# Kernel optimization log

Hardware: AMD Instinct MI355X
Metric: run time of the kernel (lower is better)

Reference implementation:

```python
import jax, jax.numpy as jnp
import numpy as np

D_CHAR, D_HID, LEN_VOC = 256, 1024, 512
BSZ, MAX_LEN = 128, 256


def setup_inputs() -> dict:
    key = jax.random.key(0)
    ks = jax.random.split(key, 14)
    s = 1.0 / np.sqrt(D_HID)  # PyTorch RNN/Linear init scale
    u = lambda k, shape: jax.random.uniform(k, shape, jnp.float32, -s, s)
    return {
        "inputs": jax.random.randint(ks[0], (BSZ, MAX_LEN), 0, LEN_VOC),
        "outputs": jax.random.randint(ks[1], (BSZ, MAX_LEN), 0, LEN_VOC),
        "emb": jax.random.normal(ks[2], (LEN_VOC, D_CHAR), jnp.float32),
        "enc_Wih": u(ks[3], (D_HID, D_CHAR)),
        "enc_Whh": u(ks[4], (D_HID, D_HID)),
        "enc_bih": u(ks[5], (D_HID,)),
        "enc_bhh": u(ks[6], (D_HID,)),
        "dec_Wih": u(ks[7], (D_HID, D_CHAR)),
        "dec_Whh": u(ks[8], (D_HID, D_HID)),
        "dec_bih": u(ks[9], (D_HID,)),
        "dec_bhh": u(ks[10], (D_HID,)),
        "out_W": u(ks[11], (LEN_VOC, D_HID)),
        "out_b": u(ks[12], (LEN_VOC,)),
    }


def rnn_scan(x_seq, h0, Wih, Whh, bih, bhh):
    """Elman RNN (tanh), batch_first input [B, T, D] -> (h_T [B,H], all h [T,B,H]).
    h_t = tanh(W_ih x_t + b_ih + W_hh h_{t-1} + b_hh), matching torch.nn.RNN."""
    # Precompute input projection for all timesteps (one big GEMM).
    xp = jnp.einsum('btd,hd->bth', x_seq, Wih) + bih + bhh  # [B,T,H]
    xp = jnp.swapaxes(xp, 0, 1)  # [T,B,H] for scan

    def step(h, x):
        h = jnp.tanh(x + h @ Whh.T)
        return h, h

    hT, hs = jax.lax.scan(step, h0, xp)
    return hT, hs


def reference(inputs, outputs, emb, enc_Wih, enc_Whh, enc_bih, enc_bhh,
              dec_Wih, dec_Whh, dec_bih, dec_bhh, out_W, out_b):
    bsz, max_len = inputs.shape
    # Encoder over input char embeddings, zero initial hidden.
    embs = emb[inputs]  # [B,T,Dc]
    h0 = jnp.zeros((bsz, D_HID), jnp.float32)
    hT, _ = rnn_scan(embs, h0, enc_Wih, enc_Whh, enc_bih, enc_bhh)
    # Teacher-forced decoder: step 0 gets zero input, step t gets emb(outputs[:, t-1]).
    dec_in = jnp.concatenate(
        [jnp.zeros((bsz, 1, D_CHAR), jnp.float32), emb[outputs[:, :-1]]], axis=1)
    _, dec_hs = rnn_scan(dec_in, hT, dec_Wih, dec_Whh, dec_bih, dec_bhh)  # [T,B,H]
    # decoder_states.transpose(0,1).view(-1, d_hid)
    states = jnp.swapaxes(dec_hs, 0, 1).reshape(-1, D_HID)  # [B*T, H]
    logits = states @ out_W.T + out_b  # [B*T, V]
    return jax.nn.log_softmax(logits, axis=1)
```

## Files before the change

### kernel.cpp

```cpp
#include <hip/hip_runtime.h>


typedef short short8 __attribute__((ext_vector_type(8)));
typedef float floatx4 __attribute__((ext_vector_type(4)));
typedef unsigned int uint4v __attribute__((ext_vector_type(4)));

#define WS_WIN    0ull
#define WS_STATES (2ull << 20)
#define WS_WB     (66ull << 20)

#define HS_STRIDE 1032

__device__ __forceinline__ float bf2f(unsigned short u) {
  union { unsigned u; float f; } x; x.u = ((unsigned)u) << 16; return x.f;
}
__device__ __forceinline__ unsigned short f2bf(float f) {
  union { float f; unsigned u; } x; x.f = f;
  unsigned r = x.u + 0x7FFFu + ((x.u >> 16) & 1u);
  return (unsigned short)(r >> 16);
}
__device__ __forceinline__ unsigned pkminu16(unsigned a, unsigned b) {
  unsigned d;
  asm("v_pk_min_u16 %0, %1, %2" : "=v"(d) : "v"(a), "v"(b));
  return d;
}

__global__ __launch_bounds__(256) void cvt_kernel(
    const float* __restrict__ src, unsigned short* __restrict__ dst, int n)
{
  const int i = (blockIdx.x * 256 + threadIdx.x) * 4;
  if (i >= n) return;
  const float4 v = *(const float4*)(src + i);
  unsigned short o[4] = {f2bf(v.x), f2bf(v.y), f2bf(v.z), f2bf(v.w)};
  *(uint2*)(dst + i) = *(const uint2*)o;
}

__global__ __launch_bounds__(256) void gemm_bt_kernel(
    const unsigned short* __restrict__ Abase,
    const int mode,
    const unsigned short* __restrict__ Bmat,
    const float* __restrict__ bias0,
    const float* __restrict__ bias1,
    unsigned short* __restrict__ outp_bf,
    float* __restrict__ outp_f,
    const int K, const int N, const int nbn)
{
  __shared__ unsigned short As[64][264];
  __shared__ unsigned short Bs[64][264];
  __shared__ const unsigned short* rowsrc[64];

  const int tid = threadIdx.x;
  const int lane = tid & 63;
  const int wave = tid >> 6;
  const int bn = blockIdx.x % nbn;
  const int bm = blockIdx.x / nbn;
  const int m0 = bm * 64;
  const int j0 = bn * 64;

  if (tid < 64) {
    const int m = m0 + tid;
    const unsigned short* src;
    if (mode == 0) {
      src = Abase + (size_t)m * K;
    } else {
      src = Abase + ((size_t)(m & 255) * 128 + (m >> 8)) * 1024;
    }
    rowsrc[tid] = src;
  }

  const floatx4 zf = {0.f, 0.f, 0.f, 0.f};
  floatx4 acc0 = zf, acc1 = zf, acc2 = zf, acc3 = zf;

  for (int kc = 0; kc < K; kc += 256) {
    __syncthreads();
#pragma unroll
    for (int i = 0; i < 8; ++i) {
      const int idx = i * 256 + tid;
      const int r = idx >> 5;
      const int c = idx & 31;
      const unsigned short* s = rowsrc[r];
      *(short8*)&As[r][c * 8] = *(const short8*)(s + kc + c * 8);
      *(short8*)&Bs[r][c * 8] =
          *(const short8*)(Bmat + (size_t)(j0 + r) * K + kc + c * 8);
    }
    __syncthreads();
    const int ar = 16 * wave + (lane & 15);
    const int kq = (lane >> 4) * 8;
#pragma unroll
    for (int kk = 0; kk < 8; ++kk) {
      const short8 a = *(const short8*)&As[ar][kk * 32 + kq];
      const short8 bv0 = *(const short8*)&Bs[(lane & 15)][kk * 32 + kq];
      acc0 = __builtin_amdgcn_mfma_f32_16x16x32_bf16(a, bv0, acc0, 0, 0, 0);
      const short8 bv1 = *(const short8*)&Bs[16 + (lane & 15)][kk * 32 + kq];
      acc1 = __builtin_amdgcn_mfma_f32_16x16x32_bf16(a, bv1, acc1, 0, 0, 0);
      const short8 bv2 = *(const short8*)&Bs[32 + (lane & 15)][kk * 32 + kq];
      acc2 = __builtin_amdgcn_mfma_f32_16x16x32_bf16(a, bv2, acc2, 0, 0, 0);
      const short8 bv3 = *(const short8*)&Bs[48 + (lane & 15)][kk * 32 + kq];
      acc3 = __builtin_amdgcn_mfma_f32_16x16x32_bf16(a, bv3, acc3, 0, 0, 0);
    }
  }

  float bs[4] = {0.f, 0.f, 0.f, 0.f};
  if (bias0) {
#pragma unroll
    for (int nt = 0; nt < 4; ++nt) {
      const int jj = j0 + nt * 16 + (lane & 15);
      bs[nt] = bias0[jj] + bias1[jj];
    }
  }
  __syncthreads();
  const int rbase = 16 * wave + (lane >> 4) * 4;
  const int cl = lane & 15;

  if (outp_bf) {
#pragma unroll
    for (int i = 0; i < 4; ++i) {
      As[rbase + i][cl]      = f2bf(acc0[i] + bs[0]);
      As[rbase + i][16 + cl] = f2bf(acc1[i] + bs[1]);
      As[rbase + i][32 + cl] = f2bf(acc2[i] + bs[2]);
      As[rbase + i][48 + cl] = f2bf(acc3[i] + bs[3]);
    }
    __syncthreads();
#pragma unroll
    for (int i = 0; i < 2; ++i) {
      const int idx = i * 256 + tid;
      const int r = idx >> 3;
      const int c = idx & 7;
      *(short8*)(outp_bf + (size_t)(m0 + r) * N + j0 + c * 8) =
          *(const short8*)&As[r][c * 8];
    }
  } else {
    float (*Asf)[66] = (float(*)[66]) & As[0][0];
#pragma unroll
    for (int i = 0; i < 4; ++i) {
      Asf[rbase + i][cl]      = acc0[i] + bs[0];
      Asf[rbase + i][16 + cl] = acc1[i] + bs[1];
      Asf[rbase + i][32 + cl] = acc2[i] + bs[2];
      Asf[rbase + i][48 + cl] = acc3[i] + bs[3];
    }
    __syncthreads();
#pragma unroll
    for (int i = 0; i < 4; ++i) {
      const int idx = i * 256 + tid;
      const int r = idx >> 4;
      const int c = idx & 15;
      *(float4*)(outp_f + (size_t)(m0 + r) * N + j0 + c * 4) =
          *(const float4*)&Asf[r][c * 4];
    }
  }
}

__global__ __launch_bounds__(512) void rnn_scan6_kernel(
    const unsigned short* __restrict__ WhhE,
    const unsigned short* __restrict__ WhhD,
    const unsigned short* __restrict__ projE,
    const unsigned short* __restrict__ projD,
    const float* __restrict__ decBih,
    const float* __restrict__ decBhh,
    const int* __restrict__ intoks,
    const int* __restrict__ outtoks,
    unsigned short* __restrict__ win,
    unsigned short* __restrict__ states)
{
  __shared__ unsigned short hs[2 * 16 * HS_STRIDE];
  __shared__ int toks[16 * 257];

  const int tid = threadIdx.x;
  const int lane = tid & 63;
  const int wave = tid >> 6;
  const int g = blockIdx.x & 7;
  const int slot = blockIdx.x >> 3;
  const int b0 = g * 16;
  const int q = lane >> 4;
  const int cl = lane & 15;
  const int jwb = slot * 128 + wave * 16;
  const int jq4 = jwb + q * 4;
  const int prow = tid >> 5;
  const int pcc = tid & 31;
  const int pc32 = pcc * 32;
  const bool own = ((pcc >> 2) == slot);

  short8 w[32];
  const floatx4 zf = {0.f, 0.f, 0.f, 0.f};
  unsigned long long obp = 0;
  const size_t prodoff = (size_t)(b0 + cl) * 1024 + jq4;

  for (int phase = 0; phase < 2; ++phase) {
    const unsigned short* Whh = phase ? WhhD : WhhE;
    const unsigned short* proj = phase ? projD : projE;
    const int* gt = phase ? outtoks : intoks;
    {
      const unsigned short* wp = Whh + (size_t)(jwb + cl) * 1024 + q * 8;
#pragma unroll
      for (int kk = 0; kk < 32; ++kk) w[kk] = *(const short8*)(wp + kk * 32);
    }
    float xb[4] = {0.f, 0.f, 0.f, 0.f};
    if (phase) {
#pragma unroll
      for (int i = 0; i < 4; ++i) xb[i] = decBih[jq4 + i] + decBhh[jq4 + i];
    }
    __syncthreads();
#pragma unroll
    for (int i = 0; i < 8; ++i) {
      const int idx = i * 512 + tid;
      toks[(idx >> 8) * 257 + (idx & 255)] =
          gt[(size_t)(b0 + (idx >> 8)) * 256 + (idx & 255)];
    }
    __syncthreads();

    for (int t = 0; t < 256; ++t) {
      const int s = phase * 256 + t;
      float xpf[4];
      {
        const int tt = phase ? (t > 0 ? t - 1 : 0) : t;
        const int tok = toks[cl * 257 + tt];
        const uint2 xr = *(const uint2*)(proj + (size_t)tok * 1024 + jq4);
        const unsigned short* xs = (const unsigned short*)&xr;
#pragma unroll
        for (int i = 0; i < 4; ++i) xpf[i] = bf2f(xs[i]);
        if (phase && t == 0) {
#pragma unroll
          for (int i = 0; i < 4; ++i) xpf[i] = xb[i];
        }
      }

      unsigned short* hsb = hs + (s & 1) * (16 * HS_STRIDE);
      if (s > 0) {
        const unsigned short* hprev =
            win + (size_t)((s - 1) & 7) * 131072 + b0 * 1024;
        if (!own) {
          const unsigned long long paddr =
              (unsigned long long)(hprev + prow * 1024 + pc32);
          uint4v d0, d1, d2, d3;
          for (;;) {
            asm volatile(
                "global_load_dwordx4 %0, %4, off sc0 sc1\n\t"
                "global_load_dwordx4 %1, %4, off offset:16 sc0 sc1\n\t"
                "global_load_dwordx4 %2, %4, off offset:32 sc0 sc1\n\t"
                "global_load_dwordx4 %3, %4, off offset:48 sc0 sc1\n\t"
                "s_waitcnt vmcnt(0)"
                : "=&v"(d0), "=&v"(d1), "=&v"(d2), "=&v"(d3)
                : "v"(paddr)
                : "memory");
            unsigned m0v = 0xFFFFFFFFu, m1v = 0xFFFFFFFFu;
            unsigned m2v = 0xFFFFFFFFu, m3v = 0xFFFFFFFFu;
#pragma unroll
            for (int i = 0; i < 4; ++i) {
              m0v = pkminu16(m0v, d0[i] ^ 0xAAAAAAAAu);
              m1v = pkminu16(m1v, d1[i] ^ 0xAAAAAAAAu);
              m2v = pkminu16(m2v, d2[i] ^ 0xAAAAAAAAu);
              m3v = pkminu16(m3v, d3[i] ^ 0xAAAAAAAAu);
            }
            const unsigned mm = pkminu16(pkminu16(m0v, m1v), pkminu16(m2v, m3v));
            const unsigned hz = (mm - 0x00010001u) & ~mm & 0x80008000u;
            if (hz == 0u) break;
            __builtin_amdgcn_s_sleep(1);
          }
          unsigned short* dst = &hsb[prow * HS_STRIDE + pc32];
          *(uint4v*)(dst + 0)  = d0;
          *(uint4v*)(dst + 8)  = d1;
          *(uint4v*)(dst + 16) = d2;
          *(uint4v*)(dst + 24) = d3;
        }
        *(unsigned long long*)&hsb[cl * HS_STRIDE + jq4] = obp;
      }
      __builtin_amdgcn_sched_barrier(0);
      asm volatile("s_waitcnt lgkmcnt(0)" ::: "memory");
      __builtin_amdgcn_s_barrier();
      __builtin_amdgcn_sched_barrier(0);

      floatx4 acc0 = zf, acc1 = zf, acc2 = zf, acc3 = zf;
      if (s > 0) {
        const unsigned short* hrow = &hsb[cl * HS_STRIDE + q * 8];
#pragma unroll
        for (int kk = 0; kk < 32; kk += 4) {
          const short8 a0 = *(const short8*)(hrow + (kk + 0) * 32);
          const short8 a1 = *(const short8*)(hrow + (kk + 1) * 32);
          const short8 a2 = *(const short8*)(hrow + (kk + 2) * 32);
          const short8 a3 = *(const short8*)(hrow + (kk + 3) * 32);
          acc0 = __builtin_amdgcn_mfma_f32_16x16x32_bf16(w[kk + 0], a0, acc0, 0, 0, 0);
          acc1 = __builtin_amdgcn_mfma_f32_16x16x32_bf16(w[kk + 1], a1, acc1, 0, 0, 0);
          acc2 = __builtin_amdgcn_mfma_f32_16x16x32_bf16(w[kk + 2], a2, acc2, 0, 0, 0);
          acc3 = __builtin_amdgcn_mfma_f32_16x16x32_bf16(w[kk + 3], a3, acc3, 0, 0, 0);
        }
      }
      unsigned short ob[4];
#pragma unroll
      for (int i = 0; i < 4; ++i) {
        const float pre = acc0[i] + acc1[i] + acc2[i] + acc3[i] + xpf[i];
        const float e = __expf(2.f * pre);
        ob[i] = f2bf(1.f - 2.f / (e + 1.f));
        if (ob[i] == 0xAAAAu) ob[i] = 0xAAABu;
      }
      obp = *(const unsigned long long*)ob;
      __hip_atomic_store(
          (unsigned long long*)(win + (size_t)(s & 7) * 131072 + prodoff),
          obp, __ATOMIC_RELAXED, __HIP_MEMORY_SCOPE_AGENT);
      if (phase) {
        __builtin_nontemporal_store(
            obp, (unsigned long long*)(states + (size_t)t * 131072 + prodoff));
      }
      if (s >= 2) {
        __hip_atomic_store(
            (unsigned long long*)(win + (size_t)((s - 2) & 7) * 131072 + prodoff),
            0xAAAAAAAAAAAAAAAAull, __ATOMIC_RELAXED, __HIP_MEMORY_SCOPE_AGENT);
      }
    }
  }
}

__global__ __launch_bounds__(256) void logsoftmax_kernel(
    float* __restrict__ logits, const float* __restrict__ outb)
{
  const int row = blockIdx.x * 4 + (threadIdx.x >> 6);
  const int lane = threadIdx.x & 63;
  float* rp = logits + (size_t)row * 512 + lane * 8;
  const float4 a0 = *(const float4*)rp;
  const float4 a1 = *(const float4*)(rp + 4);
  const float4 b0 = *(const float4*)(outb + lane * 8);
  const float4 b1 = *(const float4*)(outb + lane * 8 + 4);
  float v[8] = {a0.x + b0.x, a0.y + b0.y, a0.z + b0.z, a0.w + b0.w,
                a1.x + b1.x, a1.y + b1.y, a1.z + b1.z, a1.w + b1.w};
  float mx = v[0];
#pragma unroll
  for (int i = 1; i < 8; ++i) mx = fmaxf(mx, v[i]);
#pragma unroll
  for (int m = 1; m < 64; m <<= 1) mx = fmaxf(mx, __shfl_xor(mx, m, 64));
  float sum = 0.f;
#pragma unroll
  for (int i = 0; i < 8; ++i) sum += __expf(v[i] - mx);
#pragma unroll
  for (int m = 1; m < 64; m <<= 1) sum += __shfl_xor(sum, m, 64);
  const float lse = mx + __logf(sum);
  float4 o0 = {v[0] - lse, v[1] - lse, v[2] - lse, v[3] - lse};
  float4 o1 = {v[4] - lse, v[5] - lse, v[6] - lse, v[7] - lse};
  *(float4*)rp = o0;
  *(float4*)(rp + 4) = o1;
}

extern "C" void kernel_launch(void* const* d_in, const int* in_sizes, int n_in,
                              void* d_out, int out_size, void* d_ws, size_t ws_size,
                              hipStream_t stream)
{
  const int* inputs  = (const int*)d_in[0];
  const int* outputs = (const int*)d_in[1];
  const float* emb    = (const float*)d_in[2];
  const float* encWih = (const float*)d_in[3];
  const float* encWhh = (const float*)d_in[4];
  const float* encBih = (const float*)d_in[5];
  const float* encBhh = (const float*)d_in[6];
  const float* decWih = (const float*)d_in[7];
  const float* decWhh = (const float*)d_in[8];
  const float* decBih = (const float*)d_in[9];
  const float* decBhh = (const float*)d_in[10];
  const float* outW   = (const float*)d_in[11];
  const float* outB   = (const float*)d_in[12];

  char* ws = (char*)d_ws;
  unsigned short* win    = (unsigned short*)(ws + WS_WIN);
  unsigned short* states = (unsigned short*)(ws + WS_STATES);
  char* wb = ws + WS_WB;
  unsigned short* embB  = (unsigned short*)(wb + 0);
  unsigned short* eWihB = (unsigned short*)(wb + (512ull << 10));
  unsigned short* dWihB = (unsigned short*)(wb + (1ull << 20));
  unsigned short* eWhhB = (unsigned short*)(wb + (2ull << 20));
  unsigned short* dWhhB = (unsigned short*)(wb + (4ull << 20));
  unsigned short* outWB = (unsigned short*)(wb + (6ull << 20));
  unsigned short* projE = (unsigned short*)(wb + (7ull << 20));
  unsigned short* projD = (unsigned short*)(wb + (8ull << 20));
  float* logits = (float*)d_out;

  cvt_kernel<<<128, 256, 0, stream>>>(emb, embB, 512 * 256);
  cvt_kernel<<<256, 256, 0, stream>>>(encWih, eWihB, 1024 * 256);
  cvt_kernel<<<256, 256, 0, stream>>>(decWih, dWihB, 1024 * 256);
  cvt_kernel<<<1024, 256, 0, stream>>>(encWhh, eWhhB, 1024 * 1024);
  cvt_kernel<<<1024, 256, 0, stream>>>(decWhh, dWhhB, 1024 * 1024);
  cvt_kernel<<<512, 256, 0, stream>>>(outW, outWB, 512 * 1024);

  gemm_bt_kernel<<<128, 256, 0, stream>>>(embB, 0, eWihB, encBih, encBhh,
                                          projE, nullptr, 256, 1024, 16);
  gemm_bt_kernel<<<128, 256, 0, stream>>>(embB, 0, dWihB, decBih, decBhh,
                                          projD, nullptr, 256, 1024, 16);

  rnn_scan6_kernel<<<64, 512, 0, stream>>>(eWhhB, dWhhB, projE, projD,
                                           decBih, decBhh, inputs, outputs,
                                           win, states);

  gemm_bt_kernel<<<4096, 256, 0, stream>>>(states, 3, outWB, nullptr, nullptr,
                                           nullptr, logits, 1024, 512, 8);
  logsoftmax_kernel<<<8192, 256, 0, stream>>>(logits, outB);
}
```

Baseline: 1.830 ms.

## Halve scan block to 256 threads with two weight tiles per wave

The recurrent scan kernel now runs 4 waves per block instead of 8. Each wave holds two 16-row slices of Whh in registers and computes two output tiles, sharing each loaded h fragment across both MFMA chains. The cross-block polling of the previous hidden state now uses 8 loads per thread instead of 4, and the compute section runs at raised wave priority. Fewer waves should make each per-step barrier cheaper, at the cost of doubled register pressure (64 short8 weight registers per lane) and more serial work per wave.

```diff
diff --git a/kernel.cpp b/kernel.cpp
--- a/kernel.cpp
+++ b/kernel.cpp
@@ -150,7 +150,7 @@
   }
 }
 
-__global__ __launch_bounds__(512) void rnn_scan6_kernel(
+__global__ __launch_bounds__(256, 1) void rnn_scan7_kernel(
     const unsigned short* __restrict__ WhhE,
     const unsigned short* __restrict__ WhhD,
     const unsigned short* __restrict__ projE,
@@ -173,36 +173,44 @@
   const int b0 = g * 16;
   const int q = lane >> 4;
   const int cl = lane & 15;
-  const int jwb = slot * 128 + wave * 16;
-  const int jq4 = jwb + q * 4;
-  const int prow = tid >> 5;
-  const int pcc = tid & 31;
-  const int pc32 = pcc * 32;
-  const bool own = ((pcc >> 2) == slot);
-
-  short8 w[32];
+  const int jwb = slot * 128 + wave * 32;
+  const int jq0 = jwb + q * 4;
+  const int jq1 = jwb + 16 + q * 4;
+  const int prow = tid & 15;
+  const int pseg = tid >> 4;
+  const bool own = ((pseg >> 1) == slot);
+
+  short8 w0[32], w1[32];
   const floatx4 zf = {0.f, 0.f, 0.f, 0.f};
-  unsigned long long obp = 0;
-  const size_t prodoff = (size_t)(b0 + cl) * 1024 + jq4;
+  unsigned long long obp0 = 0, obp1 = 0;
+  const size_t prodoff0 = (size_t)(b0 + cl) * 1024 + jq0;
+  const size_t prodoff1 = (size_t)(b0 + cl) * 1024 + jq1;
 
   for (int phase = 0; phase < 2; ++phase) {
     const unsigned short* Whh = phase ? WhhD : WhhE;
     const unsigned short* proj = phase ? projD : projE;
     const int* gt = phase ? outtoks : intoks;
     {
-      const unsigned short* wp = Whh + (size_t)(jwb + cl) * 1024 + q * 8;
-#pragma unroll
-      for (int kk = 0; kk < 32; ++kk) w[kk] = *(const short8*)(wp + kk * 32);
-    }
-    float xb[4] = {0.f, 0.f, 0.f, 0.f};
+      const unsigned short* wp0 = Whh + (size_t)(jwb + cl) * 1024 + q * 8;
+      const unsigned short* wp1 = Whh + (size_t)(jwb + 16 + cl) * 1024 + q * 8;
+#pragma unroll
+      for (int kk = 0; kk < 32; ++kk) {
+        w0[kk] = *(const short8*)(wp0 + kk * 32);
+        w1[kk] = *(const short8*)(wp1 + kk * 32);
+      }
+    }
+    float xb0[4], xb1[4];
     if (phase) {
 #pragma unroll
-      for (int i = 0; i < 4; ++i) xb[i] = decBih[jq4 + i] + decBhh[jq4 + i];
-    }
-    __syncthreads();
-#pragma unroll
-    for (int i = 0; i < 8; ++i) {
-      const int idx = i * 512 + tid;
+      for (int i = 0; i < 4; ++i) {
+        xb0[i] = decBih[jq0 + i] + decBhh[jq0 + i];
+        xb1[i] = decBih[jq1 + i] + decBhh[jq1 + i];
+      }
+    }
+    __syncthreads();
+#pragma unroll
+    for (int i = 0; i < 16; ++i) {
+      const int idx = i * 256 + tid;
       toks[(idx >> 8) * 257 + (idx & 255)] =
           gt[(size_t)(b0 + (idx >> 8)) * 256 + (idx & 255)];
     }
@@ -210,100 +218,122 @@
 
     for (int t = 0; t < 256; ++t) {
       const int s = phase * 256 + t;
-      float xpf[4];
+      float xpf0[4], xpf1[4];
       {
         const int tt = phase ? (t > 0 ? t - 1 : 0) : t;
         const int tok = toks[cl * 257 + tt];
-        const uint2 xr = *(const uint2*)(proj + (size_t)tok * 1024 + jq4);
-        const unsigned short* xs = (const unsigned short*)&xr;
-#pragma unroll
-        for (int i = 0; i < 4; ++i) xpf[i] = bf2f(xs[i]);
+        const uint2 xr0 = *(const uint2*)(proj + (size_t)tok * 1024 + jq0);
+        const uint2 xr1 = *(const uint2*)(proj + (size_t)tok * 1024 + jq1);
+        const unsigned short* xs0 = (const unsigned short*)&xr0;
+        const unsigned short* xs1 = (const unsigned short*)&xr1;
+#pragma unroll
+        for (int i = 0; i < 4; ++i) { xpf0[i] = bf2f(xs0[i]); xpf1[i] = bf2f(xs1[i]); }
         if (phase && t == 0) {
 #pragma unroll
-          for (int i = 0; i < 4; ++i) xpf[i] = xb[i];
+          for (int i = 0; i < 4; ++i) { xpf0[i] = xb0[i]; xpf1[i] = xb1[i]; }
         }
       }
 
       unsigned short* hsb = hs + (s & 1) * (16 * HS_STRIDE);
       if (s > 0) {
-        const unsigned short* hprev =
-            win + (size_t)((s - 1) & 7) * 131072 + b0 * 1024;
+        *(unsigned long long*)&hsb[cl * HS_STRIDE + jq0] = obp0;
+        *(unsigned long long*)&hsb[cl * HS_STRIDE + jq1] = obp1;
         if (!own) {
+          const unsigned short* hprev =
+              win + (size_t)((s - 1) & 7) * 131072 + b0 * 1024;
           const unsigned long long paddr =
-              (unsigned long long)(hprev + prow * 1024 + pc32);
-          uint4v d0, d1, d2, d3;
+              (unsigned long long)(hprev + prow * 1024 + pseg * 64);
+          uint4v p0, p1, p2, p3, p4, p5, p6, p7;
           for (;;) {
             asm volatile(
-                "global_load_dwordx4 %0, %4, off sc0 sc1\n\t"
-                "global_load_dwordx4 %1, %4, off offset:16 sc0 sc1\n\t"
-                "global_load_dwordx4 %2, %4, off offset:32 sc0 sc1\n\t"
-                "global_load_dwordx4 %3, %4, off offset:48 sc0 sc1\n\t"
+                "global_load_dwordx4 %0, %8, off sc0 sc1\n\t"
+                "global_load_dwordx4 %1, %8, off offset:16 sc0 sc1\n\t"
+                "global_load_dwordx4 %2, %8, off offset:32 sc0 sc1\n\t"
+                "global_load_dwordx4 %3, %8, off offset:48 sc0 sc1\n\t"
+                "global_load_dwordx4 %4, %8, off offset:64 sc0 sc1\n\t"
+                "global_load_dwordx4 %5, %8, off offset:80 sc0 sc1\n\t"
+                "global_load_dwordx4 %6, %8, off offset:96 sc0 sc1\n\t"
+                "global_load_dwordx4 %7, %8, off offset:112 sc0 sc1\n\t"
                 "s_waitcnt vmcnt(0)"
-                : "=&v"(d0), "=&v"(d1), "=&v"(d2), "=&v"(d3)
+                : "=&v"(p0), "=&v"(p1), "=&v"(p2), "=&v"(p3),
+                  "=&v"(p4), "=&v"(p5), "=&v"(p6), "=&v"(p7)
                 : "v"(paddr)
                 : "memory");
             unsigned m0v = 0xFFFFFFFFu, m1v = 0xFFFFFFFFu;
             unsigned m2v = 0xFFFFFFFFu, m3v = 0xFFFFFFFFu;
 #pragma unroll
             for (int i = 0; i < 4; ++i) {
-              m0v = pkminu16(m0v, d0[i] ^ 0xAAAAAAAAu);
-              m1v = pkminu16(m1v, d1[i] ^ 0xAAAAAAAAu);
-              m2v = pkminu16(m2v, d2[i] ^ 0xAAAAAAAAu);
-              m3v = pkminu16(m3v, d3[i] ^ 0xAAAAAAAAu);
+              m0v = pkminu16(m0v, pkminu16(p0[i] ^ 0xAAAAAAAAu, p4[i] ^ 0xAAAAAAAAu));
+              m1v = pkminu16(m1v, pkminu16(p1[i] ^ 0xAAAAAAAAu, p5[i] ^ 0xAAAAAAAAu));
+              m2v = pkminu16(m2v, pkminu16(p2[i] ^ 0xAAAAAAAAu, p6[i] ^ 0xAAAAAAAAu));
+              m3v = pkminu16(m3v, pkminu16(p3[i] ^ 0xAAAAAAAAu, p7[i] ^ 0xAAAAAAAAu));
             }
             const unsigned mm = pkminu16(pkminu16(m0v, m1v), pkminu16(m2v, m3v));
             const unsigned hz = (mm - 0x00010001u) & ~mm & 0x80008000u;
             if (hz == 0u) break;
             __builtin_amdgcn_s_sleep(1);
           }
-          unsigned short* dst = &hsb[prow * HS_STRIDE + pc32];
-          *(uint4v*)(dst + 0)  = d0;
-          *(uint4v*)(dst + 8)  = d1;
-          *(uint4v*)(dst + 16) = d2;
-          *(uint4v*)(dst + 24) = d3;
+          unsigned short* dst = &hsb[prow * HS_STRIDE + pseg * 64];
+          *(uint4v*)(dst + 0)  = p0; *(uint4v*)(dst + 8)  = p1;
+          *(uint4v*)(dst + 16) = p2; *(uint4v*)(dst + 24) = p3;
+          *(uint4v*)(dst + 32) = p4; *(uint4v*)(dst + 40) = p5;
+          *(uint4v*)(dst + 48) = p6; *(uint4v*)(dst + 56) = p7;
         }
-        *(unsigned long long*)&hsb[cl * HS_STRIDE + jq4] = obp;
       }
       __builtin_amdgcn_sched_barrier(0);
       asm volatile("s_waitcnt lgkmcnt(0)" ::: "memory");
       __builtin_amdgcn_s_barrier();
       __builtin_amdgcn_sched_barrier(0);
-
-      floatx4 acc0 = zf, acc1 = zf, acc2 = zf, acc3 = zf;
+      __builtin_amdgcn_s_setprio(1);
+
+      floatx4 a00 = zf, a01 = zf, a10 = zf, a11 = zf;
       if (s > 0) {
         const unsigned short* hrow = &hsb[cl * HS_STRIDE + q * 8];
 #pragma unroll
-        for (int kk = 0; kk < 32; kk += 4) {
-          const short8 a0 = *(const short8*)(hrow + (kk + 0) * 32);
-          const short8 a1 = *(const short8*)(hrow + (kk + 1) * 32);
-          const short8 a2 = *(const short8*)(hrow + (kk + 2) * 32);
-          const short8 a3 = *(const short8*)(hrow + (kk + 3) * 32);
-          acc0 = __builtin_amdgcn_mfma_f32_16x16x32_bf16(w[kk + 0], a0, acc0, 0, 0, 0);
-          acc1 = __builtin_amdgcn_mfma_f32_16x16x32_bf16(w[kk + 1], a1, acc1, 0, 0, 0);
-          acc2 = __builtin_amdgcn_mfma_f32_16x16x32_bf16(w[kk + 2], a2, acc2, 0, 0, 0);
-          acc3 = __builtin_amdgcn_mfma_f32_16x16x32_bf16(w[kk + 3], a3, acc3, 0, 0, 0);
+        for (int kk = 0; kk < 32; kk += 2) {
+          const short8 h0 = *(const short8*)(hrow + (kk + 0) * 32);
+          const short8 h1 = *(const short8*)(hrow + (kk + 1) * 32);
+          a00 = __builtin_amdgcn_mfma_f32_16x16x32_bf16(w0[kk + 0], h0, a00, 0, 0, 0);
+          a10 = __builtin_amdgcn_mfma_f32_16x16x32_bf16(w1[kk + 0], h0, a10, 0, 0, 0);
+          a01 = __builtin_amdgcn_mfma_f32_16x16x32_bf16(w0[kk + 1], h1, a01, 0, 0, 0);
+          a11 = __builtin_amdgcn_mfma_f32_16x16x32_bf16(w1[kk + 1], h1, a11, 0, 0, 0);
         }
       }
-      unsigned short ob[4];
+      unsigned short ob[8];
 #pragma unroll
       for (int i = 0; i < 4; ++i) {
-        const float pre = acc0[i] + acc1[i] + acc2[i] + acc3[i] + xpf[i];
-        const float e = __expf(2.f * pre);
-        ob[i] = f2bf(1.f - 2.f / (e + 1.f));
+        const float pre0 = a00[i] + a01[i] + xpf0[i];
+        const float pre1 = a10[i] + a11[i] + xpf1[i];
+        const float e0 = __expf(2.f * pre0);
+        const float e1 = __expf(2.f * pre1);
+        ob[i]     = f2bf(1.f - 2.f / (e0 + 1.f));
+        ob[4 + i] = f2bf(1.f - 2.f / (e1 + 1.f));
         if (ob[i] == 0xAAAAu) ob[i] = 0xAAABu;
-      }
-      obp = *(const unsigned long long*)ob;
-      __hip_atomic_store(
-          (unsigned long long*)(win + (size_t)(s & 7) * 131072 + prodoff),
-          obp, __ATOMIC_RELAXED, __HIP_MEMORY_SCOPE_AGENT);
+        if (ob[4 + i] == 0xAAAAu) ob[4 + i] = 0xAAABu;
+      }
+      obp0 = *(const unsigned long long*)&ob[0];
+      obp1 = *(const unsigned long long*)&ob[4];
+      unsigned long long* wbase =
+          (unsigned long long*)(win + (size_t)(s & 7) * 131072);
+      __hip_atomic_store((unsigned long long*)((unsigned short*)wbase + prodoff0),
+                         obp0, __ATOMIC_RELAXED, __HIP_MEMORY_SCOPE_AGENT);
+      __hip_atomic_store((unsigned long long*)((unsigned short*)wbase + prodoff1),
+                         obp1, __ATOMIC_RELAXED, __HIP_MEMORY_SCOPE_AGENT);
+      __builtin_amdgcn_s_setprio(0);
       if (phase) {
         __builtin_nontemporal_store(
-            obp, (unsigned long long*)(states + (size_t)t * 131072 + prodoff));
+            obp0, (unsigned long long*)(states + (size_t)t * 131072 + prodoff0));
+        __builtin_nontemporal_store(
+            obp1, (unsigned long long*)(states + (size_t)t * 131072 + prodoff1));
       }
       if (s >= 2) {
-        __hip_atomic_store(
-            (unsigned long long*)(win + (size_t)((s - 2) & 7) * 131072 + prodoff),
-            0xAAAAAAAAAAAAAAAAull, __ATOMIC_RELAXED, __HIP_MEMORY_SCOPE_AGENT);
+        unsigned short* pb = win + (size_t)((s - 2) & 7) * 131072;
+        __hip_atomic_store((unsigned long long*)(pb + prodoff0),
+                           0xAAAAAAAAAAAAAAAAull, __ATOMIC_RELAXED,
+                           __HIP_MEMORY_SCOPE_AGENT);
+        __hip_atomic_store((unsigned long long*)(pb + prodoff1),
+                           0xAAAAAAAAAAAAAAAAull, __ATOMIC_RELAXED,
+                           __HIP_MEMORY_SCOPE_AGENT);
       }
     }
   }
@@ -382,7 +412,7 @@
   gemm_bt_kernel<<<128, 256, 0, stream>>>(embB, 0, dWihB, decBih, decBhh,
                                           projD, nullptr, 256, 1024, 16);
 
-  rnn_scan6_kernel<<<64, 512, 0, stream>>>(eWhhB, dWhhB, projE, projD,
+  rnn_scan7_kernel<<<64, 256, 0, stream>>>(eWhhB, dWhhB, projE, projD,
                                            decBih, decBhh, inputs, outputs,
                                            win, states);
 
```

Result: slower. 2.406 ms (+31.4%).
